# Optimization experiments

Measured on AMD Instinct MI355X. Metric: run time of the kernel, lower is better.

Reference implementation:

```python
import jax, jax.numpy as jnp
from jax import lax
import numpy as np

BETA = 0.25
K = 64   # num_embeddings
D = 64   # embedding_dim (must equal K per module's view(-1, D))
HID = 128
RES = 64
N_RES = 2


def _conv(x, w, b=None, stride=1, pad=0):
    y = lax.conv_general_dilated(x, w, (stride, stride), [(pad, pad), (pad, pad)],
                                 dimension_numbers=('NCHW', 'OIHW', 'NCHW'))
    if b is not None:
        y = y + b[None, :, None, None]
    return y


def _deconv(x, w, b, stride, pad):
    # torch ConvTranspose2d weight is (Cin, Cout, k, k); emulate via lhs-dilated conv with flipped kernel
    k = w.shape[2]
    p = k - 1 - pad
    w2 = jnp.transpose(w[:, :, ::-1, ::-1], (1, 0, 2, 3))  # -> (Cout, Cin, k, k)
    y = lax.conv_general_dilated(x, w2, (1, 1), [(p, p), (p, p)], lhs_dilation=(stride, stride),
                                 dimension_numbers=('NCHW', 'OIHW', 'NCHW'))
    return y + b[None, :, None, None]


def _res_block(x, w1, w2):
    # [Residual_Layer]*N_RES shares ONE set of weights; in-place ReLU means skip adds relu(x)
    for _ in range(N_RES):
        r = jax.nn.relu(x)
        h = _conv(r, w1, pad=1)
        h = jax.nn.relu(h)
        h = _conv(h, w2)
        x = r + h
    return jax.nn.relu(x)


def setup_inputs() -> dict:
    key = jax.random.key(0)
    ks = jax.random.split(key, 16)
    f32 = jnp.float32
    s = 0.05
    inp = {
        'x': jax.random.normal(ks[0], (32, 1, 256, 256), f32),
        # encoder
        'enc_c1_w': jax.random.normal(ks[1], (HID // 2, 1, 4, 4), f32) * s,
        'enc_c1_b': jnp.zeros((HID // 2,), f32),
        'enc_c2_w': jax.random.normal(ks[2], (HID, HID // 2, 4, 4), f32) * s,
        'enc_c2_b': jnp.zeros((HID,), f32),
        'enc_c3_w': jax.random.normal(ks[3], (HID, HID, 3, 3), f32) * s,
        'enc_c3_b': jnp.zeros((HID,), f32),
        'enc_r1_w': jax.random.normal(ks[4], (RES, HID, 3, 3), f32) * s,
        'enc_r2_w': jax.random.normal(ks[5], (HID, RES, 1, 1), f32) * s,
        # pre-VQ 1x1 conv: hidden -> K channels
        'vqc_w': jax.random.normal(ks[6], (K, HID, 1, 1), f32) * s,
        'vqc_b': jnp.zeros((K,), f32),
        # codebook, uniform(-1/K, 1/K)
        'emb': jax.random.uniform(ks[7], (K, D), f32, -1.0 / K, 1.0 / K),
        # decoder (ConvTranspose2d weights are (Cin, Cout, k, k))
        'dec_c1_w': jax.random.normal(ks[8], (D, HID, 3, 3), f32) * s,
        'dec_c1_b': jnp.zeros((HID,), f32),
        'dec_r1_w': jax.random.normal(ks[9], (RES, HID, 3, 3), f32) * s,
        'dec_r2_w': jax.random.normal(ks[10], (HID, RES, 1, 1), f32) * s,
        'dec_c2_w': jax.random.normal(ks[11], (HID, HID // 2, 4, 4), f32) * s,
        'dec_c2_b': jnp.zeros((HID // 2,), f32),
        'dec_c3_w': jax.random.normal(ks[12], (HID // 2, 1, 4, 4), f32) * s,
        'dec_c3_b': jnp.zeros((1,), f32),
    }
    return inp


def reference(x, enc_c1_w, enc_c1_b, enc_c2_w, enc_c2_b, enc_c3_w, enc_c3_b,
              enc_r1_w, enc_r2_w, vqc_w, vqc_b, emb,
              dec_c1_w, dec_c1_b, dec_r1_w, dec_r2_w, dec_c2_w, dec_c2_b, dec_c3_w, dec_c3_b):
    # ---- encoder ----
    h = jax.nn.relu(_conv(x, enc_c1_w, enc_c1_b, stride=2, pad=1))
    h = jax.nn.relu(_conv(h, enc_c2_w, enc_c2_b, stride=2, pad=1))
    h = _conv(h, enc_c3_w, enc_c3_b, pad=1)
    h = _res_block(h, enc_r1_w, enc_r2_w)
    z = _conv(h, vqc_w, vqc_b)  # (B, K, 64, 64)

    # ---- VQ ----
    zt = jnp.transpose(z, (0, 2, 3, 1))            # (B, H, W, D)
    flat = zt.reshape(-1, D)                        # (N, D)
    dist = (jnp.sum(flat ** 2, axis=1, keepdims=True)
            + jnp.sum(emb ** 2, axis=1)
            - 2.0 * flat @ emb.T)                   # (N, K)
    idx = jnp.argmin(dist, axis=1)                  # (N,)
    onehot = jax.nn.one_hot(idx, K, dtype=flat.dtype)
    q = (onehot @ emb).reshape(zt.shape)
    commitment = jnp.mean((lax.stop_gradient(q) - zt) ** 2)
    embedding_l = jnp.mean((q - lax.stop_gradient(zt)) ** 2)
    loss = commitment * BETA + embedding_l
    q_st = zt + lax.stop_gradient(q - zt)           # straight-through
    mean_enc = jnp.mean(onehot, axis=0)
    perplexity = jnp.exp(-jnp.sum(mean_enc * jnp.log(mean_enc + 1e-10)))
    qn = jnp.transpose(q_st, (0, 3, 1, 2))          # (B, D, 64, 64)

    # ---- decoder ----
    d = _deconv(qn, dec_c1_w, dec_c1_b, 1, 1)
    d = _res_block(d, dec_r1_w, dec_r2_w)
    d = jax.nn.relu(_deconv(d, dec_c2_w, dec_c2_b, 2, 1))
    x_re = jnp.tanh(_deconv(d, dec_c3_w, dec_c3_b, 2, 1))
    return (loss, x_re, perplexity, qn)
```

## Files before the change

kernel.cpp:

```cpp
#include <hip/hip_runtime.h>
#include <cmath>


static constexpr int NPOS  = 131072;
static constexpr long long NELEM = 8388608;

typedef __attribute__((ext_vector_type(8))) short short8;
typedef __attribute__((ext_vector_type(8))) unsigned short ushort8;
typedef __attribute__((ext_vector_type(4))) float f32x4;

__device__ __forceinline__ unsigned short f2bf(float f) {
  unsigned int x = __float_as_uint(f);
  unsigned int r = (x + 0x7fffu + ((x >> 16) & 1u)) >> 16;
  return (unsigned short)r;
}
__device__ __forceinline__ float bf2f(unsigned short u) {
  return __uint_as_float(((unsigned int)u) << 16);
}
__device__ __forceinline__ void split2(float v, unsigned short& h, unsigned short& l) {
  unsigned short hh = f2bf(v);
  h = hh;
  l = f2bf(v - bf2f(hh));
}

__global__ void __launch_bounds__(256) enc1_t(
    const float* __restrict__ in, const float* __restrict__ w,
    const float* __restrict__ bias,
    unsigned short* __restrict__ outh, unsigned short* __restrict__ outl)
{
  int tid = threadIdx.x;
  int rr = tid >> 7, ox = tid & 127;
  int oy  = blockIdx.x * 2 + rr;
  int oc0 = blockIdx.y * 16;
  int b   = blockIdx.z;

  const float* pl = in + (size_t)b * 65536;
  float v[16];
  #pragma unroll
  for (int ky = 0; ky < 4; ++ky) {
    int iy = 2 * oy - 1 + ky;
    #pragma unroll
    for (int kx = 0; kx < 4; ++kx) {
      int ix = 2 * ox - 1 + kx;
      v[ky * 4 + kx] = (iy >= 0 && iy < 256 && ix >= 0 && ix < 256)
                       ? pl[iy * 256 + ix] : 0.f;
    }
  }
  float acc[16];
  #pragma unroll
  for (int o = 0; o < 16; ++o) acc[o] = bias[oc0 + o];
  #pragma unroll
  for (int t = 0; t < 16; ++t)
    #pragma unroll
    for (int o = 0; o < 16; ++o)
      acc[o] += v[t] * w[(size_t)(oc0 + o) * 16 + t];

  size_t o = ((size_t)b * 16900 + (size_t)(oy + 1) * 130 + (ox + 1)) * 64 + oc0;
  ushort8 h0, h1, l0, l1;
  #pragma unroll
  for (int k = 0; k < 8; ++k) {
    unsigned short hh, ll;
    split2(fmaxf(acc[k], 0.f), hh, ll);      h0[k] = hh; l0[k] = ll;
    split2(fmaxf(acc[k + 8], 0.f), hh, ll);  h1[k] = hh; l1[k] = ll;
  }
  *(ushort8*)(outh + o)     = h0;
  *(ushort8*)(outh + o + 8) = h1;
  *(ushort8*)(outl + o)     = l0;
  *(ushort8*)(outl + o + 8) = l1;
}

template<int IC, int OC, int MODE, bool BIAS, bool RELU>
__global__ void __launch_bounds__(256) mfma_enc(
    const unsigned short* __restrict__ inh, const unsigned short* __restrict__ inl,
    const unsigned short* __restrict__ wh, const unsigned short* __restrict__ wl,
    const float* __restrict__ bias,
    const unsigned short* __restrict__ skh, const unsigned short* __restrict__ skl,
    unsigned short* __restrict__ outh, unsigned short* __restrict__ outl)
{
  constexpr int OM = OC / 16;
  constexpr int NT = (MODE == 0) ? 9 : ((MODE == 1) ? 16 : 1);
  constexpr int IW = (MODE == 1) ? 130 : 66;
  const int in_ss  = IW * IW * IC;
  const int out_ss = 4356 * OC;
  const int tid = threadIdx.x;
  const int wv = tid >> 6, lane = tid & 63;
  const int quad = lane >> 4, l15 = lane & 15;
  const int b = blockIdx.z;
  const int y = blockIdx.x * 4 + wv;
  int xs[4];
  #pragma unroll
  for (int j = 0; j < 4; ++j) xs[j] = j * 16 + l15;
  const unsigned short* ibh = inh + (size_t)b * in_ss;
  const unsigned short* ibl = inl + (size_t)b * in_ss;

  f32x4 acc[OM][4];
  #pragma unroll
  for (int m = 0; m < OM; ++m) {
    const int oc0 = m * 16 + quad * 4;
    f32x4 ini = {0.f, 0.f, 0.f, 0.f};
    if (BIAS) {
      float4 bs = *(const float4*)(bias + oc0);
      ini[0] = bs.x; ini[1] = bs.y; ini[2] = bs.z; ini[3] = bs.w;
    }
    #pragma unroll
    for (int j = 0; j < 4; ++j) {
      f32x4 a = ini;
      if (MODE == 2) {
        size_t s = (size_t)b * out_ss + ((size_t)(y + 1) * 66 + (xs[j] + 1)) * OC + oc0;
        ushort4 sh = *(const ushort4*)(skh + s);
        ushort4 sl = *(const ushort4*)(skl + s);
        a[0] += bf2f(sh.x) + bf2f(sl.x);
        a[1] += bf2f(sh.y) + bf2f(sl.y);
        a[2] += bf2f(sh.z) + bf2f(sl.z);
        a[3] += bf2f(sh.w) + bf2f(sl.w);
      }
      acc[m][j] = a;
    }
  }

  for (int t = 0; t < NT; ++t) {
    int off[4];
    #pragma unroll
    for (int j = 0; j < 4; ++j) {
      if (MODE == 1)
        off[j] = ((2 * y + (t >> 2)) * 130 + (2 * xs[j] + (t & 3))) * IC;
      else if (MODE == 0) {
        int dy = t / 3 - 1, dx = t % 3 - 1;
        off[j] = ((y + dy + 1) * 66 + (xs[j] + dx + 1)) * IC;
      } else
        off[j] = ((y + 1) * 66 + (xs[j] + 1)) * IC;
    }
    const unsigned short* wrh = wh + (size_t)t * OC * IC + l15 * IC + quad * 8;
    const unsigned short* wrl = wl + (size_t)t * OC * IC + l15 * IC + quad * 8;
    #pragma unroll
    for (int k0 = 0; k0 < IC; k0 += 32) {
      short8 bh[4], bl[4];
      #pragma unroll
      for (int j = 0; j < 4; ++j) {
        bh[j] = *(const short8*)(ibh + off[j] + quad * 8 + k0);
        bl[j] = *(const short8*)(ibl + off[j] + quad * 8 + k0);
      }
      #pragma unroll
      for (int m = 0; m < OM; ++m) {
        short8 ah = *(const short8*)(wrh + (size_t)m * 16 * IC + k0);
        short8 al = *(const short8*)(wrl + (size_t)m * 16 * IC + k0);
        #pragma unroll
        for (int j = 0; j < 4; ++j) {
          acc[m][j] = __builtin_amdgcn_mfma_f32_16x16x32_bf16(ah, bh[j], acc[m][j], 0, 0, 0);
          acc[m][j] = __builtin_amdgcn_mfma_f32_16x16x32_bf16(ah, bl[j], acc[m][j], 0, 0, 0);
          acc[m][j] = __builtin_amdgcn_mfma_f32_16x16x32_bf16(al, bh[j], acc[m][j], 0, 0, 0);
        }
      }
    }
  }

  #pragma unroll
  for (int m = 0; m < OM; ++m) {
    const int oc0 = m * 16 + quad * 4;
    #pragma unroll
    for (int j = 0; j < 4; ++j) {
      size_t o = (size_t)b * out_ss + ((size_t)(y + 1) * 66 + (xs[j] + 1)) * OC + oc0;
      ushort4 h4, l4;
      unsigned short hh, ll;
      float v;
      v = acc[m][j][0]; if (RELU) v = fmaxf(v, 0.f); split2(v, hh, ll); h4.x = hh; l4.x = ll;
      v = acc[m][j][1]; if (RELU) v = fmaxf(v, 0.f); split2(v, hh, ll); h4.y = hh; l4.y = ll;
      v = acc[m][j][2]; if (RELU) v = fmaxf(v, 0.f); split2(v, hh, ll); h4.z = hh; l4.z = ll;
      v = acc[m][j][3]; if (RELU) v = fmaxf(v, 0.f); split2(v, hh, ll); h4.w = hh; l4.w = ll;
      *(ushort4*)(outh + o) = h4;
      *(ushort4*)(outl + o) = l4;
    }
  }
}

__global__ void __launch_bounds__(256, 2) vq_k(
    const unsigned short* __restrict__ xh, const unsigned short* __restrict__ xl,
    const float* __restrict__ vw, const float* __restrict__ vb,
    const float* __restrict__ emb,
    float* __restrict__ qn, unsigned short* __restrict__ dqb,
    float* __restrict__ sum_sq, int* __restrict__ hist)
{
  int tid = threadIdx.x;
  int n = blockIdx.x * 256 + tid;
  int b = n >> 12;
  int pos = n & 4095;
  int u = pos >> 6, v2 = pos & 63;

  float z[64];
  #pragma unroll
  for (int k = 0; k < 64; ++k) z[k] = vb[k];

  size_t ibase = ((size_t)b * 4356 + (size_t)(u + 1) * 66 + (v2 + 1)) * 128;
  for (int c0 = 0; c0 < 128; c0 += 8) {
    ushort8 hh = *(const ushort8*)(xh + ibase + c0);
    ushort8 ll = *(const ushort8*)(xl + ibase + c0);
    #pragma unroll
    for (int j = 0; j < 8; ++j) {
      float v = bf2f(hh[j]) + bf2f(ll[j]);
      #pragma unroll
      for (int k = 0; k < 64; ++k) z[k] += v * vw[k * 128 + c0 + j];
    }
  }

  float z2 = 0.f;
  #pragma unroll
  for (int d = 0; d < 64; ++d) z2 += z[d] * z[d];

  float best = INFINITY;
  int bidx = 0;
  for (int k = 0; k < 64; ++k) {
    float dot = 0.f, e2 = 0.f;
    #pragma unroll
    for (int d = 0; d < 64; ++d) {
      float e = emb[k * 64 + d];
      dot += z[d] * e;
      e2  += e * e;
    }
    float dist = z2 + e2 - 2.f * dot;
    if (dist < best) { best = dist; bidx = k; }
  }

  float sq = 0.f;
  const float* eb = emb + bidx * 64;
  float* qb = qn + (size_t)b * 262144 + pos;
  unsigned short* dq = dqb + (size_t)b * 278784 + ((size_t)(u + 1) * 66 + (v2 + 1)) * 64;
  #pragma unroll
  for (int d = 0; d < 64; ++d) {
    float e = eb[d];
    float df = e - z[d];
    sq += df * df;
    qb[(size_t)d * 4096] = e;
    dq[d] = f2bf(e);
  }

  __shared__ float red[256];
  __shared__ int lh[64];
  red[tid] = sq;
  if (tid < 64) lh[tid] = 0;
  __syncthreads();
  atomicAdd(&lh[bidx], 1);
  for (int s = 128; s > 0; s >>= 1) {
    if (tid < s) red[tid] += red[tid + s];
    __syncthreads();
  }
  if (tid == 0) atomicAdd(sum_sq, red[0]);
  if (tid < 64) atomicAdd(&hist[tid], lh[tid]);
}

template<int IC, int OC, int MODE, bool HAS_BIAS, bool HAS_SKIP, bool RELU>
__global__ void __launch_bounds__(256) mfma_conv(
    const unsigned short* __restrict__ in, const unsigned short* __restrict__ wt,
    const float* __restrict__ bias, const unsigned short* __restrict__ skip,
    unsigned short* __restrict__ out, int ry, int rx, int in_ss, int out_ss)
{
  constexpr int OM = OC / 16;
  constexpr int NT = (MODE == 0) ? 9 : ((MODE == 1) ? 4 : 1);
  const int tid = threadIdx.x;
  const int wv = tid >> 6, lane = tid & 63;
  const int quad = lane >> 4, l15 = lane & 15;
  const int b = blockIdx.z;
  const int y = blockIdx.x * 4 + wv;
  int xs[4];
  #pragma unroll
  for (int j = 0; j < 4; ++j) xs[j] = j * 16 + l15;
  const unsigned short* inb = in + (size_t)b * (size_t)in_ss;

  f32x4 acc[OM][4];
  #pragma unroll
  for (int m = 0; m < OM; ++m) {
    const int oc0 = m * 16 + quad * 4;
    f32x4 ini = {0.f, 0.f, 0.f, 0.f};
    if (HAS_BIAS) {
      float4 bs = *(const float4*)(bias + oc0);
      ini[0] = bs.x; ini[1] = bs.y; ini[2] = bs.z; ini[3] = bs.w;
    }
    #pragma unroll
    for (int j = 0; j < 4; ++j) {
      f32x4 a = ini;
      if (HAS_SKIP) {
        size_t s = (size_t)b * (size_t)out_ss + ((size_t)(y + 1) * 66 + (xs[j] + 1)) * OC + oc0;
        ushort4 sv = *(const ushort4*)(skip + s);
        a[0] += bf2f(sv.x); a[1] += bf2f(sv.y); a[2] += bf2f(sv.z); a[3] += bf2f(sv.w);
      }
      acc[m][j] = a;
    }
  }

  #pragma unroll
  for (int t = 0; t < NT; ++t) {
    const int dy = (MODE == 0) ? (t / 3 - 1) : ((MODE == 1) ? (ry - (t >> 1)) : 0);
    const int dx = (MODE == 0) ? (t % 3 - 1) : ((MODE == 1) ? (rx - (t & 1)) : 0);
    const unsigned short* wr = wt + (size_t)t * OC * IC + (size_t)l15 * IC + quad * 8;
    #pragma unroll
    for (int k0 = 0; k0 < IC; k0 += 32) {
      short8 fb[4];
      #pragma unroll
      for (int j = 0; j < 4; ++j)
        fb[j] = *(const short8*)(inb + ((size_t)(y + dy + 1) * 66 + (xs[j] + dx + 1)) * IC + quad * 8 + k0);
      #pragma unroll
      for (int m = 0; m < OM; ++m) {
        short8 fa = *(const short8*)(wr + (size_t)m * 16 * IC + k0);
        #pragma unroll
        for (int j = 0; j < 4; ++j)
          acc[m][j] = __builtin_amdgcn_mfma_f32_16x16x32_bf16(fa, fb[j], acc[m][j], 0, 0, 0);
      }
    }
  }

  #pragma unroll
  for (int m = 0; m < OM; ++m) {
    const int oc0 = m * 16 + quad * 4;
    #pragma unroll
    for (int j = 0; j < 4; ++j) {
      unsigned short* o = out + (size_t)b * (size_t)out_ss
                        + ((size_t)(y + 1) * 66 + (xs[j] + 1)) * OC + oc0;
      ushort4 u4;
      float v;
      v = acc[m][j][0]; if (RELU) v = fmaxf(v, 0.f); u4.x = f2bf(v);
      v = acc[m][j][1]; if (RELU) v = fmaxf(v, 0.f); u4.y = f2bf(v);
      v = acc[m][j][2]; if (RELU) v = fmaxf(v, 0.f); u4.z = f2bf(v);
      v = acc[m][j][3]; if (RELU) v = fmaxf(v, 0.f); u4.w = f2bf(v);
      *(ushort4*)o = u4;
    }
  }
}

__global__ void __launch_bounds__(256) dec3_t(
    const unsigned short* __restrict__ p4, const float* __restrict__ w,
    const float* __restrict__ bias, float* __restrict__ out)
{
  int tid = threadIdx.x;
  int yr = tid >> 7, x = tid & 127;
  int y  = blockIdx.x * 2 + yr;
  int b  = blockIdx.z;

  const int kt[2][2] = {{1, 3}, {0, 2}};
  const int dt[2][2] = {{1, 0}, {2, 1}};

  const unsigned short* base[9];
  #pragma unroll
  for (int dy = 0; dy < 3; ++dy) {
    int iy = y + dy - 1;
    int py = iy & 1, u = iy >> 1;
    #pragma unroll
    for (int dx = 0; dx < 3; ++dx) {
      int ix = x + dx - 1;
      int px = ix & 1, v = ix >> 1;
      base[dy * 3 + dx] = p4 + ((size_t)(b * 4 + py * 2 + px) * 4356
                                + (size_t)(u + 1) * 66 + (v + 1)) * 64;
    }
  }

  float acc[4] = {0.f, 0.f, 0.f, 0.f};
  for (int oct = 0; oct < 8; ++oct) {
    ushort8 s[9];
    #pragma unroll
    for (int t = 0; t < 9; ++t)
      s[t] = *(const ushort8*)(base[t] + oct * 8);

    #pragma unroll
    for (int j = 0; j < 8; ++j) {
      const float* wp = w + (size_t)(oct * 8 + j) * 16;
      float v9[9];
      #pragma unroll
      for (int t = 0; t < 9; ++t) v9[t] = bf2f(s[t][j]);
      #pragma unroll
      for (int ry = 0; ry < 2; ++ry)
        #pragma unroll
        for (int rx = 0; rx < 2; ++rx)
          #pragma unroll
          for (int a = 0; a < 2; ++a)
            #pragma unroll
            for (int c2 = 0; c2 < 2; ++c2)
              acc[ry * 2 + rx] += v9[dt[ry][a] * 3 + dt[rx][c2]]
                                * wp[kt[ry][a] * 4 + kt[rx][c2]];
    }
  }

  float b0 = bias[0];
  float* ob = out + (size_t)b * 65536;
  #pragma unroll
  for (int ry = 0; ry < 2; ++ry)
    #pragma unroll
    for (int rx = 0; rx < 2; ++rx)
      ob[(2 * y + ry) * 256 + 2 * x + rx] = tanhf(acc[ry * 2 + rx] + b0);
}

struct RingArgs {
  unsigned short* p[5];
  int icl[5];
  int H[5];
  int planes[5];
};
__global__ void rings_k(RingArgs a)
{
  int bi = blockIdx.y;
  if ((int)blockIdx.x >= a.planes[bi]) return;
  int H = a.H[bi];
  int icl = a.icl[bi];
  int C = 1 << icl;
  unsigned short* pl = a.p[bi] + (size_t)blockIdx.x * H * H * C;
  int cells = 4 * H - 4;
  int total = cells * C;
  for (int idx = threadIdx.x; idx < total; idx += 256) {
    int cell = idx >> icl;
    int e = idx & (C - 1);
    int row, col;
    if (cell < H)             { row = 0;     col = cell; }
    else if (cell < 2 * H)    { row = H - 1; col = cell - H; }
    else if (cell < 2 * H + (H - 2)) { row = cell - 2 * H + 1; col = 0; }
    else                      { row = cell - 2 * H - (H - 2) + 1; col = H - 1; }
    pl[((size_t)row * H + col) * C + e] = 0;
  }
}

__global__ void repack_k(const float* __restrict__ c1w, const float* __restrict__ r1w,
                         const float* __restrict__ r2w, const float* __restrict__ c2w,
                         unsigned short* __restrict__ W)
{
  int idx = blockIdx.x * 256 + threadIdx.x;
  if (idx >= 286720) return;
  float val;
  if (idx < 73728) {
    int t = idx / 8192, rem = idx & 8191;
    int oc = rem >> 6, ic = rem & 63;
    int ky = t / 3, kx = t - ky * 3;
    val = c1w[((ic * 128 + oc) * 3 + (2 - ky)) * 3 + (2 - kx)];
  } else if (idx < 147456) {
    int j = idx - 73728;
    int t = j / 8192, rem = j & 8191;
    int oc = rem >> 7, ic = rem & 127;
    int ky = t / 3, kx = t - ky * 3;
    val = r1w[((oc * 128 + ic) * 3 + ky) * 3 + kx];
  } else if (idx < 155648) {
    int j = idx - 147456;
    int oc = j >> 6, ic = j & 63;
    val = r2w[oc * 64 + ic];
  } else {
    int j = idx - 155648;
    int p = j >> 15;
    int t2 = (j >> 13) & 3;
    int oc = (j >> 7) & 63;
    int ic = j & 127;
    int ry = p >> 1, rx = p & 1;
    int aY = t2 >> 1, aX = t2 & 1;
    int ky = aY ? (3 - ry) : (1 - ry);
    int kx = aX ? (3 - rx) : (1 - rx);
    val = c2w[((ic * 64 + oc) * 4 + ky) * 4 + kx];
  }
  W[idx] = f2bf(val);
}

__global__ void repack_enc_k(const float* __restrict__ c2w, const float* __restrict__ c3w,
                             const float* __restrict__ r1w, const float* __restrict__ r2w,
                             unsigned short* __restrict__ Wh, unsigned short* __restrict__ Wl)
{
  int idx = blockIdx.x * 256 + threadIdx.x;
  if (idx >= 360448) return;
  float val;
  if (idx < 131072) {
    int t = idx >> 13;
    int rem = idx & 8191;
    int oc = rem >> 6, ic = rem & 63;
    val = c2w[(((size_t)oc * 64 + ic) << 4) + t];
  } else if (idx < 278528) {
    int j = idx - 131072;
    int t = j / 16384;
    int rem = j & 16383;
    int oc = rem >> 7, ic = rem & 127;
    val = c3w[((size_t)oc * 128 + ic) * 9 + t];
  } else if (idx < 352256) {
    int j = idx - 278528;
    int t = j / 8192;
    int rem = j & 8191;
    int oc = rem >> 7, ic = rem & 127;
    val = r1w[((size_t)oc * 128 + ic) * 9 + t];
  } else {
    int j = idx - 352256;
    int oc = j >> 6, ic = j & 63;
    val = r2w[oc * 64 + ic];
  }
  unsigned short h = f2bf(val);
  Wh[idx] = h;
  Wl[idx] = f2bf(val - bf2f(h));
}

__global__ void init_k(float* sum_sq, int* hist)
{
  int t = threadIdx.x;
  if (t == 0) sum_sq[0] = 0.f;
  if (t < 64) hist[t] = 0;
}

__global__ void finalize_k(const float* __restrict__ sum_sq, const int* __restrict__ hist,
                           float* __restrict__ loss_out, float* __restrict__ perp_out)
{
  if (threadIdx.x == 0) {
    float mse = sum_sq[0] / (float)NELEM;
    loss_out[0] = 1.25f * mse;
    float ent = 0.f;
    for (int k = 0; k < 64; ++k) {
      float p = (float)hist[k] / (float)NPOS;
      ent += p * logf(p + 1e-10f);
    }
    perp_out[0] = expf(-ent);
  }
}

extern "C" void kernel_launch(void* const* d_in, const int* in_sizes, int n_in,
                              void* d_out, int out_size, void* d_ws, size_t ws_size,
                              hipStream_t stream)
{
  const float* x        = (const float*)d_in[0];
  const float* enc_c1_w = (const float*)d_in[1];
  const float* enc_c1_b = (const float*)d_in[2];
  const float* enc_c2_w = (const float*)d_in[3];
  const float* enc_c2_b = (const float*)d_in[4];
  const float* enc_c3_w = (const float*)d_in[5];
  const float* enc_c3_b = (const float*)d_in[6];
  const float* enc_r1_w = (const float*)d_in[7];
  const float* enc_r2_w = (const float*)d_in[8];
  const float* vqc_w    = (const float*)d_in[9];
  const float* vqc_b    = (const float*)d_in[10];
  const float* emb      = (const float*)d_in[11];
  const float* dec_c1_w = (const float*)d_in[12];
  const float* dec_c1_b = (const float*)d_in[13];
  const float* dec_r1_w = (const float*)d_in[14];
  const float* dec_r2_w = (const float*)d_in[15];
  const float* dec_c2_w = (const float*)d_in[16];
  const float* dec_c2_b = (const float*)d_in[17];
  const float* dec_c3_w = (const float*)d_in[18];
  const float* dec_c3_b = (const float*)d_in[19];

  float* out      = (float*)d_out;
  float* loss_out = out;
  float* xre_out  = out + 1;
  float* perp_out = out + 1 + 2097152;
  float* qn_out   = out + 2 + 2097152;

  float* sum_sq = (float*)d_ws;
  int*   hist   = (int*)d_ws + 1;
  char*  pool   = (char*)d_ws + 1024;

  unsigned short* Wd  = (unsigned short*)(pool + 0);
  unsigned short* Weh = (unsigned short*)(pool + 600000);
  unsigned short* Wel = (unsigned short*)(pool + 1400000);
  unsigned short* E1h = (unsigned short*)(pool + 2200000);
  unsigned short* E1l = (unsigned short*)(pool + 71500000);
  unsigned short* B2h = (unsigned short*)(pool + 141000000);
  unsigned short* B2l = (unsigned short*)(pool + 177000000);
  unsigned short* R0h = (unsigned short*)(pool + 2200000);
  unsigned short* R0l = (unsigned short*)(pool + 38000000);
  unsigned short* Hh  = (unsigned short*)(pool + 74000000);
  unsigned short* Hl  = (unsigned short*)(pool + 92000000);
  unsigned short* X1h = (unsigned short*)(pool + 141000000);
  unsigned short* X1l = (unsigned short*)(pool + 177000000);
  unsigned short* X2h = (unsigned short*)(pool + 2200000);
  unsigned short* X2l = (unsigned short*)(pool + 38000000);
  unsigned short* Dq  = (unsigned short*)(pool + 213000000);
  unsigned short* Y1  = (unsigned short*)(pool + 141000000);
  unsigned short* S   = (unsigned short*)(pool + 110000000);
  unsigned short* Y2  = (unsigned short*)(pool + 177000000);
  unsigned short* P4  = (unsigned short*)(pool + 2200000);

  const int SS64  = 278784;
  const int SS128 = 557568;
  const int SSP4  = 1115136;

  hipLaunchKernelGGL(init_k, dim3(1), dim3(128), 0, stream, sum_sq, hist);
  hipLaunchKernelGGL(repack_k, dim3(1120), dim3(256), 0, stream,
                     dec_c1_w, dec_r1_w, dec_r2_w, dec_c2_w, Wd);
  hipLaunchKernelGGL(repack_enc_k, dim3(1408), dim3(256), 0, stream,
                     enc_c2_w, enc_c3_w, enc_r1_w, enc_r2_w, Weh, Wel);

  {
    RingArgs a;
    a.p[0] = E1h; a.icl[0] = 6; a.H[0] = 130; a.planes[0] = 32;
    a.p[1] = E1l; a.icl[1] = 6; a.H[1] = 130; a.planes[1] = 32;
    a.p[2] = B2h; a.icl[2] = 7; a.H[2] = 66;  a.planes[2] = 32;
    a.p[3] = B2l; a.icl[3] = 7; a.H[3] = 66;  a.planes[3] = 32;
    a.p[4] = Dq;  a.icl[4] = 6; a.H[4] = 66;  a.planes[4] = 32;
    hipLaunchKernelGGL(rings_k, dim3(32, 5), dim3(256), 0, stream, a);
  }

  hipLaunchKernelGGL(enc1_t, dim3(64, 4, 32), dim3(256), 0, stream,
                     x, enc_c1_w, enc_c1_b, E1h, E1l);
  hipLaunchKernelGGL((mfma_enc<64, 128, 1, true, true>),
                     dim3(16, 1, 32), dim3(256), 0, stream,
                     E1h, E1l, Weh, Wel, enc_c2_b, nullptr, nullptr, B2h, B2l);

  {
    RingArgs a;
    a.p[0] = R0h; a.icl[0] = 7; a.H[0] = 66; a.planes[0] = 32;
    a.p[1] = R0l; a.icl[1] = 7; a.H[1] = 66; a.planes[1] = 32;
    a.p[2] = Hh;  a.icl[2] = 6; a.H[2] = 66; a.planes[2] = 32;
    a.p[3] = Hl;  a.icl[3] = 6; a.H[3] = 66; a.planes[3] = 32;
    a.p[4] = S;   a.icl[4] = 6; a.H[4] = 66; a.planes[4] = 32;
    hipLaunchKernelGGL(rings_k, dim3(32, 5), dim3(256), 0, stream, a);
  }

  hipLaunchKernelGGL((mfma_enc<128, 128, 0, true, true>),
                     dim3(16, 1, 32), dim3(256), 0, stream,
                     B2h, B2l, Weh + 131072, Wel + 131072, enc_c3_b,
                     nullptr, nullptr, R0h, R0l);

  {
    RingArgs a;
    a.p[0] = X1h; a.icl[0] = 7; a.H[0] = 66; a.planes[0] = 32;
    a.p[1] = X1l; a.icl[1] = 7; a.H[1] = 66; a.planes[1] = 32;
    a.p[2] = nullptr; a.icl[2] = 0; a.H[2] = 2; a.planes[2] = 0;
    a.p[3] = nullptr; a.icl[3] = 0; a.H[3] = 2; a.planes[3] = 0;
    a.p[4] = nullptr; a.icl[4] = 0; a.H[4] = 2; a.planes[4] = 0;
    hipLaunchKernelGGL(rings_k, dim3(32, 2), dim3(256), 0, stream, a);
  }

  hipLaunchKernelGGL((mfma_enc<128, 64, 0, false, true>),
                     dim3(16, 1, 32), dim3(256), 0, stream,
                     R0h, R0l, Weh + 278528, Wel + 278528, nullptr,
                     nullptr, nullptr, Hh, Hl);
  hipLaunchKernelGGL((mfma_enc<64, 128, 2, false, true>),
                     dim3(16, 1, 32), dim3(256), 0, stream,
                     Hh, Hl, Weh + 352256, Wel + 352256, nullptr,
                     R0h, R0l, X1h, X1l);

  {
    RingArgs a;
    a.p[0] = X2h; a.icl[0] = 7; a.H[0] = 66; a.planes[0] = 32;
    a.p[1] = X2l; a.icl[1] = 7; a.H[1] = 66; a.planes[1] = 32;
    a.p[2] = nullptr; a.icl[2] = 0; a.H[2] = 2; a.planes[2] = 0;
    a.p[3] = nullptr; a.icl[3] = 0; a.H[3] = 2; a.planes[3] = 0;
    a.p[4] = nullptr; a.icl[4] = 0; a.H[4] = 2; a.planes[4] = 0;
    hipLaunchKernelGGL(rings_k, dim3(32, 2), dim3(256), 0, stream, a);
  }

  hipLaunchKernelGGL((mfma_enc<128, 64, 0, false, true>),
                     dim3(16, 1, 32), dim3(256), 0, stream,
                     X1h, X1l, Weh + 278528, Wel + 278528, nullptr,
                     nullptr, nullptr, Hh, Hl);
  hipLaunchKernelGGL((mfma_enc<64, 128, 2, false, true>),
                     dim3(16, 1, 32), dim3(256), 0, stream,
                     Hh, Hl, Weh + 352256, Wel + 352256, nullptr,
                     X1h, X1l, X2h, X2l);

  hipLaunchKernelGGL(vq_k, dim3(512), dim3(256), 0, stream,
                     X2h, X2l, vqc_w, vqc_b, emb, qn_out, Dq, sum_sq, hist);

  {
    RingArgs a;
    a.p[0] = Y1;  a.icl[0] = 7; a.H[0] = 66; a.planes[0] = 32;
    a.p[1] = Y2;  a.icl[1] = 7; a.H[1] = 66; a.planes[1] = 32;
    a.p[2] = P4;  a.icl[2] = 6; a.H[2] = 66; a.planes[2] = 128;
    a.p[3] = nullptr; a.icl[3] = 0; a.H[3] = 2; a.planes[3] = 0;
    a.p[4] = nullptr; a.icl[4] = 0; a.H[4] = 2; a.planes[4] = 0;
    hipLaunchKernelGGL(rings_k, dim3(128, 3), dim3(256), 0, stream, a);
  }

  hipLaunchKernelGGL((mfma_conv<64, 128, 0, true, false, true>),
                     dim3(16, 1, 32), dim3(256), 0, stream,
                     Dq, Wd, dec_c1_b, nullptr, Y1, 0, 0, SS64, SS128);
  hipLaunchKernelGGL((mfma_conv<128, 64, 0, false, false, true>),
                     dim3(16, 1, 32), dim3(256), 0, stream,
                     Y1, Wd + 73728, nullptr, nullptr, S, 0, 0, SS128, SS64);
  hipLaunchKernelGGL((mfma_conv<64, 128, 2, false, true, true>),
                     dim3(16, 1, 32), dim3(256), 0, stream,
                     S, Wd + 147456, nullptr, Y1, Y2, 0, 0, SS64, SS128);
  hipLaunchKernelGGL((mfma_conv<128, 64, 0, false, false, true>),
                     dim3(16, 1, 32), dim3(256), 0, stream,
                     Y2, Wd + 73728, nullptr, nullptr, S, 0, 0, SS128, SS64);
  hipLaunchKernelGGL((mfma_conv<64, 128, 2, false, true, true>),
                     dim3(16, 1, 32), dim3(256), 0, stream,
                     S, Wd + 147456, nullptr, Y2, Y1, 0, 0, SS64, SS128);

  for (int p = 0; p < 4; ++p) {
    hipLaunchKernelGGL((mfma_conv<128, 64, 1, true, false, true>),
                       dim3(16, 1, 32), dim3(256), 0, stream,
                       Y1, Wd + 155648 + p * 32768, dec_c2_b, nullptr,
                       P4 + (size_t)p * 4356 * 64, p >> 1, p & 1, SS128, SSP4);
  }

  hipLaunchKernelGGL(dec3_t, dim3(64, 1, 32), dim3(256), 0, stream,
                     P4, dec_c3_w, dec_c3_b, xre_out);

  hipLaunchKernelGGL(finalize_k, dim3(1), dim3(64), 0, stream,
                     sum_sq, hist, loss_out, perp_out);
}
```

Baseline: 1.991 ms.

## Move VQ projection and codebook distances onto bf16x3 MFMA, merge deconv phase launches

The scalar per-thread VQ kernel, which computed the 1x1 pre-VQ conv and all 64 codebook dot products in FP32 registers, is replaced by an MFMA kernel. It uses split-bf16 (three-product) matrix ops for both the projection and the distance GEMM, stages z through shared memory, and reduces argmin and the squared error with wave shuffles. Codebook norms and the bf16 splits of the weights are precomputed by a new repack kernel. The four stride-2 deconv phase launches are also merged into one grid using blockIdx.y. The aim is to cut the heavy scalar FMA work and register pressure in the VQ step. The risk is a changed tie-break or split precision that could flip argmin choices.

After: 1.871 ms. -6.1%, faster.

```diff
diff --git a/kernel.cpp b/kernel.cpp
--- a/kernel.cpp
+++ b/kernel.cpp
@@ -173,77 +173,135 @@
   }
 }
 
-__global__ void __launch_bounds__(256, 2) vq_k(
+__global__ void __launch_bounds__(256) vq_mfma(
     const unsigned short* __restrict__ xh, const unsigned short* __restrict__ xl,
-    const float* __restrict__ vw, const float* __restrict__ vb,
-    const float* __restrict__ emb,
+    const unsigned short* __restrict__ wvh, const unsigned short* __restrict__ wvl,
+    const unsigned short* __restrict__ evh, const unsigned short* __restrict__ evl,
+    const float* __restrict__ emb, const float* __restrict__ e2,
+    const float* __restrict__ vb,
     float* __restrict__ qn, unsigned short* __restrict__ dqb,
     float* __restrict__ sum_sq, int* __restrict__ hist)
 {
-  int tid = threadIdx.x;
-  int n = blockIdx.x * 256 + tid;
-  int b = n >> 12;
-  int pos = n & 4095;
-  int u = pos >> 6, v2 = pos & 63;
-
-  float z[64];
-  #pragma unroll
-  for (int k = 0; k < 64; ++k) z[k] = vb[k];
-
-  size_t ibase = ((size_t)b * 4356 + (size_t)(u + 1) * 66 + (v2 + 1)) * 128;
-  for (int c0 = 0; c0 < 128; c0 += 8) {
-    ushort8 hh = *(const ushort8*)(xh + ibase + c0);
-    ushort8 ll = *(const ushort8*)(xl + ibase + c0);
+  __shared__ float zsh[4][16][65];
+  __shared__ int lh[64];
+  const int tid = threadIdx.x;
+  const int wv = tid >> 6, lane = tid & 63;
+  const int quad = lane >> 4, l15 = lane & 15;
+  const int y = blockIdx.x;
+  const int b = blockIdx.z;
+  const int x = wv * 16 + l15;
+  if (tid < 64) lh[tid] = 0;
+
+  f32x4 zacc[4];
+  #pragma unroll
+  for (int m = 0; m < 4; ++m) {
+    float4 bv = *(const float4*)(vb + m * 16 + quad * 4);
+    zacc[m][0] = bv.x; zacc[m][1] = bv.y; zacc[m][2] = bv.z; zacc[m][3] = bv.w;
+  }
+  size_t xoff = ((size_t)b * 4356 + (size_t)(y + 1) * 66 + (x + 1)) * 128;
+  #pragma unroll
+  for (int k0 = 0; k0 < 128; k0 += 32) {
+    short8 bh = *(const short8*)(xh + xoff + k0 + quad * 8);
+    short8 bl = *(const short8*)(xl + xoff + k0 + quad * 8);
+    #pragma unroll
+    for (int m = 0; m < 4; ++m) {
+      short8 ah = *(const short8*)(wvh + (size_t)(m * 16 + l15) * 128 + k0 + quad * 8);
+      short8 al = *(const short8*)(wvl + (size_t)(m * 16 + l15) * 128 + k0 + quad * 8);
+      zacc[m] = __builtin_amdgcn_mfma_f32_16x16x32_bf16(ah, bh, zacc[m], 0, 0, 0);
+      zacc[m] = __builtin_amdgcn_mfma_f32_16x16x32_bf16(ah, bl, zacc[m], 0, 0, 0);
+      zacc[m] = __builtin_amdgcn_mfma_f32_16x16x32_bf16(al, bh, zacc[m], 0, 0, 0);
+    }
+  }
+
+  float z2p = 0.f;
+  #pragma unroll
+  for (int m = 0; m < 4; ++m)
+    #pragma unroll
+    for (int r = 0; r < 4; ++r) {
+      float zv = zacc[m][r];
+      zsh[wv][l15][m * 16 + quad * 4 + r] = zv;
+      z2p += zv * zv;
+    }
+  z2p += __shfl_xor(z2p, 16);
+  z2p += __shfl_xor(z2p, 32);
+  __syncthreads();
+
+  f32x4 dacc[4];
+  #pragma unroll
+  for (int m = 0; m < 4; ++m) { dacc[m][0]=0.f; dacc[m][1]=0.f; dacc[m][2]=0.f; dacc[m][3]=0.f; }
+  #pragma unroll
+  for (int k0 = 0; k0 < 64; k0 += 32) {
+    short8 bh, bl;
     #pragma unroll
     for (int j = 0; j < 8; ++j) {
-      float v = bf2f(hh[j]) + bf2f(ll[j]);
-      #pragma unroll
-      for (int k = 0; k < 64; ++k) z[k] += v * vw[k * 128 + c0 + j];
-    }
-  }
-
-  float z2 = 0.f;
-  #pragma unroll
-  for (int d = 0; d < 64; ++d) z2 += z[d] * z[d];
+      float zv = zsh[wv][l15][k0 + quad * 8 + j];
+      unsigned short hh, ll;
+      split2(zv, hh, ll);
+      bh[j] = (short)hh; bl[j] = (short)ll;
+    }
+    #pragma unroll
+    for (int m = 0; m < 4; ++m) {
+      short8 ah = *(const short8*)(evh + (size_t)(m * 16 + l15) * 64 + k0 + quad * 8);
+      short8 al = *(const short8*)(evl + (size_t)(m * 16 + l15) * 64 + k0 + quad * 8);
+      dacc[m] = __builtin_amdgcn_mfma_f32_16x16x32_bf16(ah, bh, dacc[m], 0, 0, 0);
+      dacc[m] = __builtin_amdgcn_mfma_f32_16x16x32_bf16(ah, bl, dacc[m], 0, 0, 0);
+      dacc[m] = __builtin_amdgcn_mfma_f32_16x16x32_bf16(al, bh, dacc[m], 0, 0, 0);
+    }
+  }
 
   float best = INFINITY;
-  int bidx = 0;
-  for (int k = 0; k < 64; ++k) {
-    float dot = 0.f, e2 = 0.f;
-    #pragma unroll
-    for (int d = 0; d < 64; ++d) {
-      float e = emb[k * 64 + d];
-      dot += z[d] * e;
-      e2  += e * e;
-    }
-    float dist = z2 + e2 - 2.f * dot;
-    if (dist < best) { best = dist; bidx = k; }
-  }
-
+  int bidx = 64;
+  #pragma unroll
+  for (int m = 0; m < 4; ++m) {
+    float4 e2v = *(const float4*)(e2 + m * 16 + quad * 4);
+    #pragma unroll
+    for (int r = 0; r < 4; ++r) {
+      float e2s = (r == 0) ? e2v.x : (r == 1) ? e2v.y : (r == 2) ? e2v.z : e2v.w;
+      float d = z2p + e2s - 2.f * dacc[m][r];
+      int code = m * 16 + quad * 4 + r;
+      if (d < best || (d == best && code < bidx)) { best = d; bidx = code; }
+    }
+  }
+  {
+    float ob = __shfl_xor(best, 16);
+    int   oi = __shfl_xor(bidx, 16);
+    if (ob < best || (ob == best && oi < bidx)) { best = ob; bidx = oi; }
+    ob = __shfl_xor(best, 32);
+    oi = __shfl_xor(bidx, 32);
+    if (ob < best || (ob == best && oi < bidx)) { best = ob; bidx = oi; }
+  }
+
+  float ev[16];
+  #pragma unroll
+  for (int i = 0; i < 4; ++i) {
+    float4 t = *(const float4*)(emb + (size_t)bidx * 64 + quad * 16 + i * 4);
+    ev[i * 4] = t.x; ev[i * 4 + 1] = t.y; ev[i * 4 + 2] = t.z; ev[i * 4 + 3] = t.w;
+  }
   float sq = 0.f;
-  const float* eb = emb + bidx * 64;
-  float* qb = qn + (size_t)b * 262144 + pos;
-  unsigned short* dq = dqb + (size_t)b * 278784 + ((size_t)(u + 1) * 66 + (v2 + 1)) * 64;
-  #pragma unroll
-  for (int d = 0; d < 64; ++d) {
-    float e = eb[d];
-    float df = e - z[d];
+  #pragma unroll
+  for (int i = 0; i < 16; ++i) {
+    float zv = zsh[wv][l15][quad * 16 + i];
+    float df = ev[i] - zv;
     sq += df * df;
-    qb[(size_t)d * 4096] = e;
-    dq[d] = f2bf(e);
-  }
-
-  __shared__ float red[256];
-  __shared__ int lh[64];
-  red[tid] = sq;
-  if (tid < 64) lh[tid] = 0;
+  }
+  #pragma unroll
+  for (int off = 1; off < 64; off <<= 1) sq += __shfl_xor(sq, off);
+  if (lane == 0) atomicAdd(sum_sq, sq);
+  if (quad == 0) atomicAdd(&lh[bidx], 1);
+
+  int pos = y * 64 + x;
+  float* qb = qn + (size_t)b * 262144 + (size_t)(quad * 16) * 4096 + pos;
+  #pragma unroll
+  for (int i = 0; i < 16; ++i) qb[(size_t)i * 4096] = ev[i];
+
+  unsigned short* dq = dqb + ((size_t)b * 4356 + (size_t)(y + 1) * 66 + (x + 1)) * 64 + quad * 16;
+  ushort8 d0, d1;
+  #pragma unroll
+  for (int i = 0; i < 8; ++i) { d0[i] = f2bf(ev[i]); d1[i] = f2bf(ev[i + 8]); }
+  *(ushort8*)dq = d0;
+  *(ushort8*)(dq + 8) = d1;
+
   __syncthreads();
-  atomicAdd(&lh[bidx], 1);
-  for (int s = 128; s > 0; s >>= 1) {
-    if (tid < s) red[tid] += red[tid + s];
-    __syncthreads();
-  }
-  if (tid == 0) atomicAdd(sum_sq, red[0]);
   if (tid < 64) atomicAdd(&hist[tid], lh[tid]);
 }
 
@@ -251,10 +309,17 @@
 __global__ void __launch_bounds__(256) mfma_conv(
     const unsigned short* __restrict__ in, const unsigned short* __restrict__ wt,
     const float* __restrict__ bias, const unsigned short* __restrict__ skip,
-    unsigned short* __restrict__ out, int ry, int rx, int in_ss, int out_ss)
+    unsigned short* __restrict__ out, int in_ss, int out_ss)
 {
   constexpr int OM = OC / 16;
   constexpr int NT = (MODE == 0) ? 9 : ((MODE == 1) ? 4 : 1);
+  int ry = 0, rx = 0;
+  if (MODE == 1) {
+    int p = blockIdx.y;
+    ry = p >> 1; rx = p & 1;
+    wt  += (size_t)p * 4 * OC * IC;
+    out += (size_t)p * 4356 * OC;
+  }
   const int tid = threadIdx.x;
   const int wv = tid >> 6, lane = tid & 63;
   const int quad = lane >> 4, l15 = lane & 15;
@@ -485,6 +550,31 @@
   Wl[idx] = f2bf(val - bf2f(h));
 }
 
+__global__ void repack_vq_k(const float* __restrict__ vqw, const float* __restrict__ emb,
+                            unsigned short* __restrict__ wvh, unsigned short* __restrict__ wvl,
+                            unsigned short* __restrict__ evh, unsigned short* __restrict__ evl,
+                            float* __restrict__ e2)
+{
+  int idx = blockIdx.x * 256 + threadIdx.x;
+  if (idx < 8192) {
+    float v = vqw[idx];
+    unsigned short h = f2bf(v);
+    wvh[idx] = h;
+    wvl[idx] = f2bf(v - bf2f(h));
+  } else if (idx < 12288) {
+    int j = idx - 8192;
+    float v = emb[j];
+    unsigned short h = f2bf(v);
+    evh[j] = h;
+    evl[j] = f2bf(v - bf2f(h));
+  }
+  if (idx < 64) {
+    float s = 0.f;
+    for (int d = 0; d < 64; ++d) { float e = emb[idx * 64 + d]; s += e * e; }
+    e2[idx] = s;
+  }
+}
+
 __global__ void init_k(float* sum_sq, int* hist)
 {
   int t = threadIdx.x;
@@ -545,6 +635,11 @@
   unsigned short* Wd  = (unsigned short*)(pool + 0);
   unsigned short* Weh = (unsigned short*)(pool + 600000);
   unsigned short* Wel = (unsigned short*)(pool + 1400000);
+  unsigned short* Wvh = (unsigned short*)(pool + 2121728);
+  unsigned short* Wvl = (unsigned short*)(pool + 2138112);
+  unsigned short* Evh = (unsigned short*)(pool + 2154496);
+  unsigned short* Evl = (unsigned short*)(pool + 2162688);
+  float*          E2  = (float*)(pool + 2170880);
   unsigned short* E1h = (unsigned short*)(pool + 2200000);
   unsigned short* E1l = (unsigned short*)(pool + 71500000);
   unsigned short* B2h = (unsigned short*)(pool + 141000000);
@@ -572,6 +667,8 @@
                      dec_c1_w, dec_r1_w, dec_r2_w, dec_c2_w, Wd);
   hipLaunchKernelGGL(repack_enc_k, dim3(1408), dim3(256), 0, stream,
                      enc_c2_w, enc_c3_w, enc_r1_w, enc_r2_w, Weh, Wel);
+  hipLaunchKernelGGL(repack_vq_k, dim3(48), dim3(256), 0, stream,
+                     vqc_w, emb, Wvh, Wvl, Evh, Evl, E2);
 
   {
     RingArgs a;
@@ -642,8 +739,9 @@
                      Hh, Hl, Weh + 352256, Wel + 352256, nullptr,
                      X1h, X1l, X2h, X2l);
 
-  hipLaunchKernelGGL(vq_k, dim3(512), dim3(256), 0, stream,
-                     X2h, X2l, vqc_w, vqc_b, emb, qn_out, Dq, sum_sq, hist);
+  hipLaunchKernelGGL(vq_mfma, dim3(64, 1, 32), dim3(256), 0, stream,
+                     X2h, X2l, Wvh, Wvl, Evh, Evl, emb, E2, vqc_b,
+                     qn_out, Dq, sum_sq, hist);
 
   {
     RingArgs a;
@@ -657,26 +755,23 @@
 
   hipLaunchKernelGGL((mfma_conv<64, 128, 0, true, false, true>),
                      dim3(16, 1, 32), dim3(256), 0, stream,
-                     Dq, Wd, dec_c1_b, nullptr, Y1, 0, 0, SS64, SS128);
+                     Dq, Wd, dec_c1_b, nullptr, Y1, SS64, SS128);
   hipLaunchKernelGGL((mfma_conv<128, 64, 0, false, false, true>),
                      dim3(16, 1, 32), dim3(256), 0, stream,
-                     Y1, Wd + 73728, nullptr, nullptr, S, 0, 0, SS128, SS64);
+                     Y1, Wd + 73728, nullptr, nullptr, S, SS128, SS64);
   hipLaunchKernelGGL((mfma_conv<64, 128, 2, false, true, true>),
                      dim3(16, 1, 32), dim3(256), 0, stream,
-                     S, Wd + 147456, nullptr, Y1, Y2, 0, 0, SS64, SS128);
+                     S, Wd + 147456, nullptr, Y1, Y2, SS64, SS128);
   hipLaunchKernelGGL((mfma_conv<128, 64, 0, false, false, true>),
                      dim3(16, 1, 32), dim3(256), 0, stream,
-                     Y2, Wd + 73728, nullptr, nullptr, S, 0, 0, SS128, SS64);
+                     Y2, Wd + 73728, nullptr, nullptr, S, SS128, SS64);
   hipLaunchKernelGGL((mfma_conv<64, 128, 2, false, true, true>),
                      dim3(16, 1, 32), dim3(256), 0, stream,
-                     S, Wd + 147456, nullptr, Y2, Y1, 0, 0, SS64, SS128);
-
-  for (int p = 0; p < 4; ++p) {
-    hipLaunchKernelGGL((mfma_conv<128, 64, 1, true, false, true>),
-                       dim3(16, 1, 32), dim3(256), 0, stream,
-                       Y1, Wd + 155648 + p * 32768, dec_c2_b, nullptr,
-                       P4 + (size_t)p * 4356 * 64, p >> 1, p & 1, SS128, SSP4);
-  }
+                     S, Wd + 147456, nullptr, Y2, Y1, SS64, SS128);
+
+  hipLaunchKernelGGL((mfma_conv<128, 64, 1, true, false, true>),
+                     dim3(16, 4, 32), dim3(256), 0, stream,
+                     Y1, Wd + 155648, dec_c2_b, nullptr, P4, SS128, SSP4);
 
   hipLaunchKernelGGL(dec3_t, dim3(64, 1, 32), dim3(256), 0, stream,
                      P4, dec_c3_w, dec_c3_b, xre_out);
```
